# Performance work log

Measured on AMD Instinct MI355X. Metric: run time of the kernel, lower is better.

The kernel has to match this reference:

```python
import jax, jax.numpy as jnp
import numpy as np
import math

B, T_FUT, T_LOOK, D, H = 8, 512, 2048, 1024, 16
HD = D // H


def setup_inputs() -> dict:
    key = jax.random.key(0)
    ks = jax.random.split(key, 12)
    xav = 1.0 / math.sqrt(D)  # approx xavier_uniform scale for square [D,D]
    return {
        "encoded_representation": jax.random.normal(ks[0], (B, T_LOOK, D), jnp.float32),
        "future_queries": jax.random.normal(ks[1], (B, T_FUT, D), jnp.float32),
        "decoder_lengths": jax.random.randint(ks[2], (B,), 1, T_FUT + 1),
        "encoder_lengths": jax.random.randint(ks[3], (B,), 1, T_LOOK + 1),
        "wq_w": jax.random.normal(ks[4], (D, D), jnp.float32) * xav,
        "wq_b": jnp.zeros((D,), jnp.float32),
        "wk_w": jax.random.normal(ks[5], (D, D), jnp.float32) * xav,
        "wk_b": jnp.zeros((D,), jnp.float32),
        "wv_w": jax.random.normal(ks[6], (D, D), jnp.float32) * xav,
        "wv_b": jnp.zeros((D,), jnp.float32),
        "wo_w": jax.random.normal(ks[7], (D, D), jnp.float32) * xav,
        "wo_b": jnp.zeros((D,), jnp.float32),
    }


def reference(encoded_representation, future_queries, decoder_lengths, encoder_lengths,
              wq_w, wq_b, wk_w, wk_b, wv_w, wv_b, wo_w, wo_b):
    # variable-length padding mask: [B, 1, T_fut, T_look]
    dec_valid = jnp.arange(T_FUT)[None, :] < decoder_lengths[:, None]   # [B, T_fut]
    enc_valid = jnp.arange(T_LOOK)[None, :] < encoder_lengths[:, None]  # [B, T_look]
    mask = dec_valid[:, None, :, None] & enc_valid[:, None, None, :]

    # torch nn.Linear: y = x @ W^T + b
    Q = (future_queries @ wq_w.T + wq_b).reshape(B, T_FUT, H, HD)
    K = (encoded_representation @ wk_w.T + wk_b).reshape(B, T_LOOK, H, HD)
    V = (encoded_representation @ wv_w.T + wv_b).reshape(B, T_LOOK, H, HD)

    scores = jnp.einsum("bqhd,bkhd->bhqk", Q, K) / math.sqrt(HD)
    # NOTE: faithful to source, which fills masked positions with -1e-09 (not -1e9)
    scores = jnp.where(mask, scores, jnp.float32(-1e-09))
    probs = jax.nn.softmax(scores, axis=-1)

    attended = jnp.einsum("bhqk,bkhd->bqhd", probs, V).reshape(B, T_FUT, D)
    return attended @ wo_w.T + wo_b
```

## Files before the change

### kernel.cpp

```cpp
#include <hip/hip_runtime.h>

typedef __attribute__((ext_vector_type(4))) float f32x4;
typedef __attribute__((ext_vector_type(8))) short s16x8;

__device__ __forceinline__ ushort f2bf(float f) {
  unsigned u = __float_as_uint(f);
  return (ushort)((u + 0x7fffu + ((u >> 16) & 1u)) >> 16);
}

__global__ __launch_bounds__(256) void cvt_bf16(const float4* __restrict__ in,
                                                ushort* __restrict__ out, int n4) {
  int stride = gridDim.x * blockDim.x;
  for (int i = blockIdx.x * blockDim.x + threadIdx.x; i < n4; i += stride) {
    float4 v = in[i];
    uint2 o;
    o.x = (unsigned)f2bf(v.x) | ((unsigned)f2bf(v.y) << 16);
    o.y = (unsigned)f2bf(v.z) | ((unsigned)f2bf(v.w) << 16);
    *(uint2*)(out + (size_t)i * 4) = o;
  }
}

__global__ __launch_bounds__(256) void cvt_bf16_w4(const float4* __restrict__ a,
                                                   const float4* __restrict__ b,
                                                   const float4* __restrict__ c,
                                                   const float4* __restrict__ d,
                                                   ushort* __restrict__ oa, ushort* __restrict__ ob,
                                                   ushort* __restrict__ oc, ushort* __restrict__ od) {
  int idx = blockIdx.x * 256 + threadIdx.x;
  int sel = idx >> 18, k = idx & 262143;
  const float4* src = sel == 0 ? a : sel == 1 ? b : sel == 2 ? c : d;
  ushort* dst = sel == 0 ? oa : sel == 1 ? ob : sel == 2 ? oc : od;
  float4 v = src[k];
  uint2 o;
  o.x = (unsigned)f2bf(v.x) | ((unsigned)f2bf(v.y) << 16);
  o.y = (unsigned)f2bf(v.z) | ((unsigned)f2bf(v.w) << 16);
  *(uint2*)(dst + (size_t)k * 4) = o;
}

__device__ __forceinline__ void gload_lds16(const void* g, void* l) {
  __builtin_amdgcn_global_load_lds((const __attribute__((address_space(1))) void*)g,
                                   (__attribute__((address_space(3))) void*)l, 16, 0, 0);
}

__global__ __launch_bounds__(512, 1) void gemm256_kv(
    const ushort* __restrict__ A, const ushort* __restrict__ Bw,
    const float* __restrict__ biasK, const float* __restrict__ biasV,
    ushort* __restrict__ Ko, ushort* __restrict__ Vt, float* __restrict__ Tsum,
    int M, int K) {
  __shared__ char lds[131072];
  const int tid = threadIdx.x;
  const int lane = tid & 63, wid = tid >> 6;
  const int g = lane >> 4, r = lane & 15;
  const int wm = wid >> 2, wn = wid & 3;
  const int bid = blockIdx.x;
  const int xcd = bid & 7, inner = bid >> 3;
  const int m0 = (xcd * 8 + (inner & 7)) * 256;
  const int n0 = (inner >> 3) * 256;
  const size_t rowb = (size_t)K * 2;

  const int srow = tid >> 3;
  const int scb = (((tid & 7) ^ (srow & 7)) << 4);
  const char* Asrc = (const char*)A + (size_t)(m0 + srow) * rowb + scb;
  const char* Bsrc = (const char*)Bw + (size_t)(n0 + srow) * rowb + scb;

  auto sAh = [&](int kt, int h) {
    char* d0 = lds + (kt & 1) * 32768 + h * 16384 + tid * 16;
    const char* s0 = Asrc + (size_t)(h * 128) * rowb + (size_t)kt * 128;
    gload_lds16(s0, d0);
    gload_lds16(s0 + (size_t)64 * rowb, d0 + 8192);
  };
  auto sBh = [&](int kt, int h) {
    char* d0 = lds + 65536 + (kt & 1) * 32768 + h * 16384 + tid * 16;
    const char* s0 = Bsrc + (size_t)(h * 128) * rowb + (size_t)kt * 128;
    gload_lds16(s0, d0);
    gload_lds16(s0 + (size_t)64 * rowb, d0 + 8192);
  };

  const int cb0 = (g * 16) ^ ((r & 7) << 4);
  const int cb1 = (64 + g * 16) ^ ((r & 7) << 4);

  f32x4 acc[8][4] = {};

  sAh(0, 0); sAh(0, 1); sBh(0, 0); sBh(0, 1); sBh(1, 0); sBh(1, 1);
  asm volatile("s_waitcnt vmcnt(4)" ::: "memory");
  __builtin_amdgcn_s_barrier();

#define MFMA_(a, b, c) __builtin_amdgcn_mfma_f32_16x16x32_bf16(a, b, c, 0, 0, 0)
#define PH(AB, Q, STAGE, WAIT)                                                 \
  {                                                                            \
    s16x8 aq0 = *(const s16x8*)(AB + (2 * (Q)) * 2048 + cb0);                  \
    s16x8 aq1 = *(const s16x8*)(AB + (2 * (Q)) * 2048 + cb1);                  \
    s16x8 aq2 = *(const s16x8*)(AB + (2 * (Q) + 1) * 2048 + cb0);              \
    s16x8 aq3 = *(const s16x8*)(AB + (2 * (Q) + 1) * 2048 + cb1);              \
    STAGE;                                                                     \
    __builtin_amdgcn_s_barrier();                                              \
    asm volatile("s_waitcnt lgkmcnt(0)" ::: "memory");                         \
    __builtin_amdgcn_sched_barrier(0);                                         \
    __builtin_amdgcn_s_setprio(1);                                             \
    _Pragma("unroll") for (int ni = 0; ni < 4; ++ni)                           \
        acc[2 * (Q)][ni] = MFMA_(aq0, bfr[ni][0], acc[2 * (Q)][ni]);           \
    _Pragma("unroll") for (int ni = 0; ni < 4; ++ni)                           \
        acc[2 * (Q) + 1][ni] = MFMA_(aq2, bfr[ni][0], acc[2 * (Q) + 1][ni]);   \
    _Pragma("unroll") for (int ni = 0; ni < 4; ++ni)                           \
        acc[2 * (Q)][ni] = MFMA_(aq1, bfr[ni][1], acc[2 * (Q)][ni]);           \
    _Pragma("unroll") for (int ni = 0; ni < 4; ++ni)                           \
        acc[2 * (Q) + 1][ni] = MFMA_(aq3, bfr[ni][1], acc[2 * (Q) + 1][ni]);   \
    __builtin_amdgcn_s_setprio(0);                                             \
    WAIT;                                                                      \
    __builtin_amdgcn_s_barrier();                                              \
  }
#define LOADB(BB)                                                              \
  _Pragma("unroll") for (int ni = 0; ni < 4; ++ni) {                           \
    bfr[ni][0] = *(const s16x8*)(BB + ni * 2048 + cb0);                        \
    bfr[ni][1] = *(const s16x8*)(BB + ni * 2048 + cb1);                        \
  }

  const int NIT = K >> 7;
  const char* AbB = lds + wm * 16384 + r * 128;
  const char* BbB = lds + 65536 + (wn >> 1) * 16384 + (wn & 1) * 8192 + r * 128;

  for (int it = 0; it < NIT; ++it) {
    const bool st = (it + 1 < NIT);
    const int k1 = 2 * it + 1, k2 = 2 * it + 2, k3 = 2 * it + 3;
    s16x8 bfr[4][2];
    LOADB(BbB);
    PH(AbB, 0, sAh(k1, 0), );
    PH(AbB, 1, sAh(k1, 1), );
    PH(AbB, 2, if (st) sBh(k2, 0), );
    PH(AbB, 3, if (st) sBh(k2, 1),
       if (st) { asm volatile("s_waitcnt vmcnt(4)" ::: "memory"); } else {
         asm volatile("s_waitcnt vmcnt(0)" ::: "memory");
       });
    const char* Ab1 = AbB + 32768;
    const char* Bb1 = BbB + 32768;
    LOADB(Bb1);
    PH(Ab1, 0, if (st) sAh(k2, 0), );
    PH(Ab1, 1, if (st) sAh(k2, 1), );
    PH(Ab1, 2, if (st) sBh(k3, 0), );
    PH(Ab1, 3, if (st) sBh(k3, 1),
       if (st) { asm volatile("s_waitcnt vmcnt(4)" ::: "memory"); });
  }
#undef PH
#undef LOADB
#undef MFMA_

  if (n0 < 1024) {
#pragma unroll
    for (int ni = 0; ni < 4; ++ni) {
      const int col = wn * 64 + ni * 16 + r;
      const float bv = biasK[n0 + col];
#pragma unroll
      for (int i = 0; i < 8; ++i)
#pragma unroll
        for (int j = 0; j < 4; ++j) {
          const int row = wm * 128 + i * 16 + g * 4 + j;
          *(ushort*)(lds + ((row * 512 + col * 2) ^ (((row >> 2) & 7) << 4))) =
              f2bf(acc[i][ni][j] + bv);
        }
    }
    __syncthreads();
    const int c = tid & 31, r0 = tid >> 5;
#pragma unroll
    for (int u = 0; u < 16; ++u) {
      const int row = u * 16 + r0;
      s16x8 v = *(const s16x8*)(lds + ((row * 512 + c * 16) ^ (((row >> 2) & 7) << 4)));
      *(s16x8*)(Ko + (size_t)(m0 + row) * 1024 + n0 + c * 8) = v;
    }
  } else {
    const int nv0 = n0 - 1024;
    const int bb = m0 >> 11, tt0 = m0 & 2047;
#pragma unroll
    for (int ni = 0; ni < 4; ++ni) {
      const int nv = nv0 + wn * 64 + ni * 16 + r;
      const float bv = biasV[nv];
#pragma unroll
      for (int qq = 0; qq < 2; ++qq) {
        float s = 0.0f;
#pragma unroll
        for (int ii = 0; ii < 4; ++ii)
#pragma unroll
          for (int j = 0; j < 4; ++j) s += acc[qq * 4 + ii][ni][j];
        s += __shfl_xor(s, 16);
        s += __shfl_xor(s, 32);
        if (g == 0) {
          const int gt = (m0 + (wm * 2 + qq) * 64) >> 6;
          Tsum[((size_t)((gt >> 5) * 16 + (nv >> 6)) * 33 + (gt & 31)) * 64 + (nv & 63)] =
              s + 64.0f * bv;
        }
      }
    }
#pragma unroll
    for (int ni = 0; ni < 4; ++ni) {
      const int rowl = wn * 64 + ni * 16 + r;
      const float bv = biasV[nv0 + rowl];
#pragma unroll
      for (int i = 0; i < 8; ++i)
#pragma unroll
        for (int j = 0; j < 4; ++j) {
          const int coll = wm * 128 + i * 16 + g * 4 + j;
          *(ushort*)(lds + ((rowl * 512 + coll * 2) ^ ((rowl & 7) << 4))) =
              f2bf(acc[i][ni][j] + bv);
        }
    }
    __syncthreads();
    const int c = tid & 31, r0 = tid >> 5;
#pragma unroll
    for (int u = 0; u < 16; ++u) {
      const int row = u * 16 + r0;
      s16x8 v = *(const s16x8*)(lds + ((row * 512 + c * 16) ^ ((row & 7) << 4)));
      *(s16x8*)(Vt + ((size_t)bb * 1024 + nv0 + row) * 2048 + tt0 + c * 8) = v;
    }
  }
}

template <int EPI>
__global__ __launch_bounds__(256) void gemm_bt(const ushort* __restrict__ A,
                                               const ushort* __restrict__ B,
                                               const float* __restrict__ bias,
                                               void* __restrict__ Cout, float oscale,
                                               int M, int N, int K) {
  __shared__ ushort As[128 * 32];
  __shared__ ushort Bs[128 * 32];
  const int tid = threadIdx.x;
  const int lane = tid & 63, w = tid >> 6;
  const int g = lane >> 4, r = lane & 15;
  const int m0 = blockIdx.x * 128, n0 = blockIdx.y * 128;
  const int wm = (w >> 1) * 64, wn = (w & 1) * 64;

  const int srow = tid >> 2;
  const int scb = (tid & 3) * 16;
  const char* Ag = (const char*)(A + (size_t)(m0 + srow) * K) + scb;
  const char* Bg = (const char*)(B + (size_t)(n0 + srow) * K) + scb;
  char* AsB = (char*)As + (tid & 192) * 16;
  char* BsB = (char*)Bs + (tid & 192) * 16;
  const size_t rowskip = (size_t)64 * K * sizeof(ushort);

  f32x4 acc[4][4] = {};

  for (int k0 = 0; k0 < K; k0 += 32) {
    gload_lds16(Ag + (size_t)k0 * 2, AsB);
    gload_lds16(Ag + rowskip + (size_t)k0 * 2, AsB + 4096);
    gload_lds16(Bg + (size_t)k0 * 2, BsB);
    gload_lds16(Bg + rowskip + (size_t)k0 * 2, BsB + 4096);
    __syncthreads();
    s16x8 af[4], bf[4];
#pragma unroll
    for (int i = 0; i < 4; ++i) af[i] = *(const s16x8*)&As[(wm + i * 16 + r) * 32 + g * 8];
#pragma unroll
    for (int i = 0; i < 4; ++i) bf[i] = *(const s16x8*)&Bs[(wn + i * 16 + r) * 32 + g * 8];
#pragma unroll
    for (int mi = 0; mi < 4; ++mi)
#pragma unroll
      for (int ni = 0; ni < 4; ++ni)
        acc[mi][ni] =
            __builtin_amdgcn_mfma_f32_16x16x32_bf16(af[mi], bf[ni], acc[mi][ni], 0, 0, 0);
    __syncthreads();
  }

  if constexpr (EPI == 0) {
    ushort* C = (ushort*)Cout;
#pragma unroll
    for (int ni = 0; ni < 4; ++ni) {
      const int n = n0 + wn + ni * 16 + r;
      const float bv = bias[n];
#pragma unroll
      for (int mi = 0; mi < 4; ++mi) {
        const int mb = m0 + wm + mi * 16 + g * 4;
#pragma unroll
        for (int j = 0; j < 4; ++j)
          C[(size_t)(mb + j) * N + n] = f2bf((acc[mi][ni][j] + bv) * oscale);
      }
    }
  } else {
    float* C = (float*)Cout;
#pragma unroll
    for (int ni = 0; ni < 4; ++ni) {
      const int n = n0 + wn + ni * 16 + r;
      const float bv = bias[n];
#pragma unroll
      for (int mi = 0; mi < 4; ++mi) {
        const int mb = m0 + wm + mi * 16 + g * 4;
#pragma unroll
        for (int j = 0; j < 4; ++j)
          C[(size_t)(mb + j) * N + n] = acc[mi][ni][j] + bv;
      }
    }
  }
}

__global__ __launch_bounds__(64) void vsuffix(float* __restrict__ T) {
  const int bh = blockIdx.x;
  const int d = threadIdx.x;
  float* p = T + (size_t)bh * 33 * 64 + d;
  float run = 0.0f;
  p[32 * 64] = 0.0f;
  for (int t = 31; t >= 0; --t) {
    run += p[t * 64];
    p[t * 64] = run;
  }
}

__device__ __forceinline__ ushort* swz(ushort* base, int row, int colb) {
  return (ushort*)((char*)base + row * 128 + (colb ^ ((row & 7) << 4)));
}

__global__ __launch_bounds__(256) void attn_fwd(
    const ushort* __restrict__ Q, const ushort* __restrict__ Km,
    const ushort* __restrict__ Vt, const float* __restrict__ Vsuf,
    const int* __restrict__ dlen, const int* __restrict__ elen,
    ushort* __restrict__ Oatt) {
  const int tid = threadIdx.x;
  const int lane = tid & 63, w = tid >> 6;
  const int g = lane >> 4, r = lane & 15;
  const int qt = blockIdx.x, b = blockIdx.y, h = blockIdx.z;
  const int dl = dlen[b], el = elen[b];
  const float* VS = Vsuf + (size_t)(b * 16 + h) * 33 * 64;

  if (qt * 64 >= dl) {
    const int qrow = qt * 64 + w * 16 + g * 4;
#pragma unroll
    for (int dt = 0; dt < 4; ++dt) {
      const ushort hv = f2bf(VS[dt * 16 + r] * (1.0f / 2048.0f));
#pragma unroll
      for (int j = 0; j < 4; ++j)
        Oatt[(size_t)(b * 512 + qrow + j) * 1024 + h * 64 + dt * 16 + r] = hv;
    }
    return;
  }

  __shared__ ushort Ks[64 * 64];
  __shared__ ushort Vs[64 * 64];
  __shared__ ushort Ps[4 * 16 * 64];
  ushort* PsW = Ps + w * 16 * 64;
  const int qbase = qt * 64 + w * 16;

  s16x8 qf[2];
  {
    const ushort* qp = Q + (size_t)(b * 512 + qbase + r) * 1024 + h * 64 + g * 8;
    qf[0] = *(const s16x8*)qp;
    qf[1] = *(const s16x8*)(qp + 32);
  }

  f32x4 o[4] = {};
  float lrow[4] = {0.0f, 0.0f, 0.0f, 0.0f};
  bool qok[4];
#pragma unroll
  for (int j = 0; j < 4; ++j) qok[j] = (qbase + g * 4 + j) < dl;

  const int sr = tid >> 3;
  const int sc8 = (tid & 7) * 8;
  const int scb = sc8 * 2;
  const ushort* Kg = Km + (size_t)(b * 2048 + sr) * 1024 + h * 64 + sc8;
  const ushort* Vg = Vt + ((size_t)b * 1024 + h * 64 + sr) * 2048 + sc8;

  const int t_last = (el - 1) >> 6;

  s16x8 pk0, pk1, pv0, pv1;
  {
    pk0 = *(const s16x8*)(Kg);
    pk1 = *(const s16x8*)(Kg + (size_t)32 * 1024);
    pv0 = *(const s16x8*)(Vg);
    pv1 = *(const s16x8*)(Vg + (size_t)32 * 2048);
  }

  for (int t = 0; t <= t_last; ++t) {
    *(s16x8*)swz(Ks, sr, scb) = pk0;
    *(s16x8*)swz(Ks, sr + 32, scb) = pk1;
    *(s16x8*)swz(Vs, sr, scb) = pv0;
    *(s16x8*)swz(Vs, sr + 32, scb) = pv1;
    __syncthreads();

    if (t < t_last) {
      const int kv0 = (t + 1) * 64;
      pk0 = *(const s16x8*)(Kg + (size_t)kv0 * 1024);
      pk1 = *(const s16x8*)(Kg + (size_t)(kv0 + 32) * 1024);
      pv0 = *(const s16x8*)(Vg + kv0);
      pv1 = *(const s16x8*)(Vg + (size_t)32 * 2048 + kv0);
    }

    const int kv0 = t * 64;
    float p[4][4];
#pragma unroll
    for (int nt = 0; nt < 4; ++nt) {
      f32x4 s = {};
      s16x8 kf0 = *(const s16x8*)swz(Ks, nt * 16 + r, g * 16);
      s16x8 kf1 = *(const s16x8*)swz(Ks, nt * 16 + r, 64 + g * 16);
      s = __builtin_amdgcn_mfma_f32_16x16x32_bf16(qf[0], kf0, s, 0, 0, 0);
      s = __builtin_amdgcn_mfma_f32_16x16x32_bf16(qf[1], kf1, s, 0, 0, 0);
      const bool kok = (kv0 + nt * 16 + r) < el;
#pragma unroll
      for (int j = 0; j < 4; ++j) {
        const float pe = __builtin_amdgcn_exp2f(s[j]);
        p[nt][j] = (kok && qok[j]) ? pe : 1.0f;
      }
    }
#pragma unroll
    for (int nt = 0; nt < 4; ++nt)
#pragma unroll
      for (int j = 0; j < 4; ++j) lrow[j] += p[nt][j];

#pragma unroll
    for (int nt = 0; nt < 4; ++nt) {
#pragma unroll
      for (int jp = 0; jp < 4; jp += 2) {
        unsigned pk;
        asm("v_cvt_pk_bf16_f32 %0, %1, %2" : "=v"(pk) : "v"(p[nt][jp]), "v"(p[nt][jp + 1]));
        *swz(PsW, g * 4 + jp, (nt * 16 + r) * 2) = (ushort)pk;
        *swz(PsW, g * 4 + jp + 1, (nt * 16 + r) * 2) = (ushort)(pk >> 16);
      }
    }

#pragma unroll
    for (int kc = 0; kc < 2; ++kc) {
      s16x8 pf = *(const s16x8*)swz(PsW, r, kc * 64 + g * 16);
#pragma unroll
      for (int dt = 0; dt < 4; ++dt) {
        s16x8 vf = *(const s16x8*)swz(Vs, dt * 16 + r, kc * 64 + g * 16);
        o[dt] = __builtin_amdgcn_mfma_f32_16x16x32_bf16(pf, vf, o[dt], 0, 0, 0);
      }
    }
    __syncthreads();
  }

  const float tailcnt = (float)(2048 - (t_last + 1) * 64);
  const float* VT = VS + (t_last + 1) * 64;
#pragma unroll
  for (int dt = 0; dt < 4; ++dt) {
    const float tv = VT[dt * 16 + r];
#pragma unroll
    for (int j = 0; j < 4; ++j) o[dt][j] += tv;
  }

  float inv[4];
#pragma unroll
  for (int j = 0; j < 4; ++j) {
    float s = lrow[j];
    s += __shfl_xor(s, 1);
    s += __shfl_xor(s, 2);
    s += __shfl_xor(s, 4);
    s += __shfl_xor(s, 8);
    inv[j] = 1.0f / (s + tailcnt);
  }
#pragma unroll
  for (int dt = 0; dt < 4; ++dt)
#pragma unroll
    for (int j = 0; j < 4; ++j)
      Oatt[(size_t)(b * 512 + qbase + g * 4 + j) * 1024 + h * 64 + dt * 16 + r] =
          f2bf(o[dt][j] * inv[j]);
}

extern "C" void kernel_launch(void* const* d_in, const int* in_sizes, int n_in,
                              void* d_out, int out_size, void* d_ws, size_t ws_size,
                              hipStream_t stream) {
  const float* enc  = (const float*)d_in[0];
  const float* fq   = (const float*)d_in[1];
  const int* dlen   = (const int*)d_in[2];
  const int* elen   = (const int*)d_in[3];
  const float* wq_w = (const float*)d_in[4];
  const float* wq_b = (const float*)d_in[5];
  const float* wk_w = (const float*)d_in[6];
  const float* wk_b = (const float*)d_in[7];
  const float* wv_w = (const float*)d_in[8];
  const float* wv_b = (const float*)d_in[9];
  const float* wo_w = (const float*)d_in[10];
  const float* wo_b = (const float*)d_in[11];

  char* ws = (char*)d_ws;
  ushort* enc16 = (ushort*)(ws + 0);
  ushort* fq16  = (ushort*)(ws + 33554432);
  float*  Vsuf  = (float*)(ws + 33554432);
  ushort* wq16  = (ushort*)(ws + 41943040);
  ushort* wk16  = (ushort*)(ws + 44040192);
  ushort* wv16  = (ushort*)(ws + 46137344);
  ushort* wo16  = (ushort*)(ws + 48234496);
  ushort* Qw    = (ushort*)(ws + 50331648);
  ushort* Kw    = (ushort*)(ws + 58720256);
  ushort* Vtw   = (ushort*)(ws + 92274688);
  ushort* attw  = (ushort*)(ws + 125829120);

  cvt_bf16<<<2048, 256, 0, stream>>>((const float4*)enc, enc16, 16384 * 1024 / 4);
  cvt_bf16<<<1024, 256, 0, stream>>>((const float4*)fq, fq16, 4096 * 1024 / 4);
  cvt_bf16_w4<<<4096, 256, 0, stream>>>((const float4*)wq_w, (const float4*)wk_w,
                                        (const float4*)wv_w, (const float4*)wo_w,
                                        wq16, wk16, wv16, wo16);

  const float qscale = 0.125f * 1.44269504088896340736f;
  gemm_bt<0><<<dim3(32, 8), 256, 0, stream>>>(fq16, wq16, wq_b, Qw, qscale, 4096, 1024, 1024);

  gemm256_kv<<<512, 512, 0, stream>>>(enc16, wk16, wk_b, wv_b, Kw, Vtw, Vsuf, 16384, 1024);
  vsuffix<<<128, 64, 0, stream>>>(Vsuf);

  attn_fwd<<<dim3(8, 8, 16), 256, 0, stream>>>(Qw, Kw, Vtw, Vsuf, dlen, elen, attw);

  gemm_bt<2><<<dim3(32, 8), 256, 0, stream>>>(attw, wo16, wo_b, d_out, 1.0f, 4096, 1024, 1024);
}
```

Baseline: 208.2 us.

## Fuse Q projection into KV GEMM launch and skip padded row tiles

The separate Q-projection GEMM is merged into the 256x256 KV GEMM kernel by adding 64 extra blocks that compute Q with bias and softmax scale. Blocks whose row tile starts past the encoder length (K tiles) or decoder length (Q tiles) exit early, skipping work on padded rows that the attention masks out. V tiles are still always computed because the suffix sums need them. The workspace layout moves Vsuf so it no longer aliases fq16, which is now read concurrently. Uncomputed K/Q rows stay garbage, so correctness depends on the attention kernel never reading past the lengths.

```diff
diff --git a/kernel.cpp b/kernel.cpp
--- a/kernel.cpp
+++ b/kernel.cpp
@@ -42,26 +42,51 @@
                                    (__attribute__((address_space(3))) void*)l, 16, 0, 0);
 }
 
-__global__ __launch_bounds__(512, 1) void gemm256_kv(
-    const ushort* __restrict__ A, const ushort* __restrict__ Bw,
-    const float* __restrict__ biasK, const float* __restrict__ biasV,
-    ushort* __restrict__ Ko, ushort* __restrict__ Vt, float* __restrict__ Tsum,
-    int M, int K) {
+__global__ __launch_bounds__(512, 1) void gemm256_fused(
+    const ushort* __restrict__ enc16, const ushort* __restrict__ fq16,
+    const ushort* __restrict__ Bkv, const ushort* __restrict__ Bq,
+    const float* __restrict__ wk_b, const float* __restrict__ wv_b,
+    const float* __restrict__ wq_b,
+    ushort* __restrict__ Ko, ushort* __restrict__ Vt, ushort* __restrict__ Qo,
+    float* __restrict__ Tsum, const int* __restrict__ dlen,
+    const int* __restrict__ elen, float qscale) {
   __shared__ char lds[131072];
   const int tid = threadIdx.x;
   const int lane = tid & 63, wid = tid >> 6;
   const int g = lane >> 4, r = lane & 15;
   const int wm = wid >> 2, wn = wid & 3;
   const int bid = blockIdx.x;
-  const int xcd = bid & 7, inner = bid >> 3;
-  const int m0 = (xcd * 8 + (inner & 7)) * 256;
-  const int n0 = (inner >> 3) * 256;
-  const size_t rowb = (size_t)K * 2;
+
+  const ushort* Amat;
+  const ushort* Bmat;
+  int m0, n0, role;
+  if (bid < 512) {
+    const int xcd = bid & 7, inner = bid >> 3;
+    m0 = (xcd * 8 + (inner & 7)) * 256;
+    n0 = (inner >> 3) * 256;
+    Amat = enc16;
+    Bmat = Bkv;
+    if (n0 < 1024) {
+      role = 0;
+      if ((m0 & 2047) >= elen[m0 >> 11]) return;
+    } else {
+      role = 1;
+    }
+  } else {
+    const int q = bid - 512;
+    m0 = (q & 15) * 256;
+    n0 = (q >> 4) * 256;
+    Amat = fq16;
+    Bmat = Bq;
+    role = 2;
+    if ((m0 & 511) >= dlen[m0 >> 9]) return;
+  }
+  const size_t rowb = 2048;
 
   const int srow = tid >> 3;
   const int scb = (((tid & 7) ^ (srow & 7)) << 4);
-  const char* Asrc = (const char*)A + (size_t)(m0 + srow) * rowb + scb;
-  const char* Bsrc = (const char*)Bw + (size_t)(n0 + srow) * rowb + scb;
+  const char* Asrc = (const char*)Amat + (size_t)(m0 + srow) * rowb + scb;
+  const char* Bsrc = (const char*)Bmat + (size_t)(n0 + srow) * rowb + scb;
 
   auto sAh = [&](int kt, int h) {
     char* d0 = lds + (kt & 1) * 32768 + h * 16384 + tid * 16;
@@ -115,7 +140,7 @@
     bfr[ni][1] = *(const s16x8*)(BB + ni * 2048 + cb1);                        \
   }
 
-  const int NIT = K >> 7;
+  const int NIT = 8;
   const char* AbB = lds + wm * 16384 + r * 128;
   const char* BbB = lds + 65536 + (wn >> 1) * 16384 + (wn & 1) * 8192 + r * 128;
 
@@ -144,18 +169,21 @@
 #undef LOADB
 #undef MFMA_
 
-  if (n0 < 1024) {
+  if (role != 1) {
+    ushort* C = (role == 2) ? Qo : Ko;
+    const float* bias0 = (role == 2) ? wq_b : wk_b;
+    const float sc = (role == 2) ? qscale : 1.0f;
 #pragma unroll
     for (int ni = 0; ni < 4; ++ni) {
       const int col = wn * 64 + ni * 16 + r;
-      const float bv = biasK[n0 + col];
+      const float bv = bias0[n0 + col];
 #pragma unroll
       for (int i = 0; i < 8; ++i)
 #pragma unroll
         for (int j = 0; j < 4; ++j) {
           const int row = wm * 128 + i * 16 + g * 4 + j;
           *(ushort*)(lds + ((row * 512 + col * 2) ^ (((row >> 2) & 7) << 4))) =
-              f2bf(acc[i][ni][j] + bv);
+              f2bf((acc[i][ni][j] + bv) * sc);
         }
     }
     __syncthreads();
@@ -164,7 +192,7 @@
     for (int u = 0; u < 16; ++u) {
       const int row = u * 16 + r0;
       s16x8 v = *(const s16x8*)(lds + ((row * 512 + c * 16) ^ (((row >> 2) & 7) << 4)));
-      *(s16x8*)(Ko + (size_t)(m0 + row) * 1024 + n0 + c * 8) = v;
+      *(s16x8*)(C + (size_t)(m0 + row) * 1024 + n0 + c * 8) = v;
     }
   } else {
     const int nv0 = n0 - 1024;
@@ -172,7 +200,7 @@
 #pragma unroll
     for (int ni = 0; ni < 4; ++ni) {
       const int nv = nv0 + wn * 64 + ni * 16 + r;
-      const float bv = biasV[nv];
+      const float bv = wv_b[nv];
 #pragma unroll
       for (int qq = 0; qq < 2; ++qq) {
         float s = 0.0f;
@@ -192,7 +220,7 @@
 #pragma unroll
     for (int ni = 0; ni < 4; ++ni) {
       const int rowl = wn * 64 + ni * 16 + r;
-      const float bv = biasV[nv0 + rowl];
+      const float bv = wv_b[nv0 + rowl];
 #pragma unroll
       for (int i = 0; i < 8; ++i)
 #pragma unroll
@@ -468,15 +496,15 @@
   char* ws = (char*)d_ws;
   ushort* enc16 = (ushort*)(ws + 0);
   ushort* fq16  = (ushort*)(ws + 33554432);
-  float*  Vsuf  = (float*)(ws + 33554432);
+  float*  Vsuf  = (float*)(ws + 41943040 + 2097152 * 4);
   ushort* wq16  = (ushort*)(ws + 41943040);
   ushort* wk16  = (ushort*)(ws + 44040192);
   ushort* wv16  = (ushort*)(ws + 46137344);
   ushort* wo16  = (ushort*)(ws + 48234496);
-  ushort* Qw    = (ushort*)(ws + 50331648);
-  ushort* Kw    = (ushort*)(ws + 58720256);
-  ushort* Vtw   = (ushort*)(ws + 92274688);
-  ushort* attw  = (ushort*)(ws + 125829120);
+  ushort* Qw    = (ushort*)(ws + 52428800);
+  ushort* Kw    = (ushort*)(ws + 60817408);
+  ushort* Vtw   = (ushort*)(ws + 94371840);
+  ushort* attw  = (ushort*)(ws + 127926272);
 
   cvt_bf16<<<2048, 256, 0, stream>>>((const float4*)enc, enc16, 16384 * 1024 / 4);
   cvt_bf16<<<1024, 256, 0, stream>>>((const float4*)fq, fq16, 4096 * 1024 / 4);
@@ -485,9 +513,8 @@
                                         wq16, wk16, wv16, wo16);
 
   const float qscale = 0.125f * 1.44269504088896340736f;
-  gemm_bt<0><<<dim3(32, 8), 256, 0, stream>>>(fq16, wq16, wq_b, Qw, qscale, 4096, 1024, 1024);
-
-  gemm256_kv<<<512, 512, 0, stream>>>(enc16, wk16, wk_b, wv_b, Kw, Vtw, Vsuf, 16384, 1024);
+  gemm256_fused<<<576, 512, 0, stream>>>(enc16, fq16, wk16, wq16, wk_b, wv_b, wq_b,
+                                         Kw, Vtw, Qw, Vsuf, dlen, elen, qscale);
   vsuffix<<<128, 64, 0, stream>>>(Vsuf);
 
   attn_fwd<<<dim3(8, 8, 16), 256, 0, stream>>>(Qw, Kw, Vtw, Vsuf, dlen, elen, attw);
```

New measurement: 198.2 us. 1.05x faster.
